# Optimization experiments

Measured on AMD Instinct MI355X. Metric: run time of the kernel, lower is better.

Reference implementation:

```python
import jax, jax.numpy as jnp
import numpy as np

B, Q, D, H, HD, LP, M = 16, 1, 2048, 16, 128, 2048, 8192
EPS = 1e-5

def _ln(x, w, b):
    mu = jnp.mean(x, axis=-1, keepdims=True)
    var = jnp.mean((x - mu) ** 2, axis=-1, keepdims=True)
    return (x - mu) * jax.lax.rsqrt(var + EPS) * w + b

def setup_inputs() -> dict:
    key = jax.random.key(0)
    ks = jax.random.split(key, 8)
    std = 0.02
    return {
        "input": jax.random.normal(ks[0], (B, Q, D), jnp.float32),
        "past_key": jax.random.normal(ks[1], (B, LP, H, HD), jnp.float32),
        "past_value": jax.random.normal(ks[2], (B, LP, H, HD), jnp.float32),
        "ln0_w": jnp.ones((D,), jnp.float32),
        "ln0_b": jnp.zeros((D,), jnp.float32),
        "ln1_w": jnp.ones((D,), jnp.float32),
        "ln1_b": jnp.zeros((D,), jnp.float32),
        "wqkv": jax.random.normal(ks[3], (3 * D, D), jnp.float32) * std,
        "wo": jax.random.normal(ks[4], (D, D), jnp.float32) * std,
        "fc0_w": jax.random.normal(ks[5], (M, D), jnp.float32) * std,
        "fc0_b": jnp.zeros((M,), jnp.float32),
        "fc1_w": jax.random.normal(ks[6], (D, M), jnp.float32) * std,
        "fc1_b": jnp.zeros((D,), jnp.float32),
    }

def reference(input, past_key, past_value, ln0_w, ln0_b, ln1_w, ln1_b,
              wqkv, wo, fc0_w, fc0_b, fc1_w, fc1_b):
    # norm0 + fused QKV projection (no bias)
    x = _ln(input, ln0_w, ln0_b)                       # [B,Q,D]
    qkv = (x @ wqkv.T).reshape(B, Q, 3, H, HD)
    q, k, v = qkv[:, :, 0], qkv[:, :, 1], qkv[:, :, 2]  # each [B,Q,H,HD]
    # append to KV cache
    k = jnp.concatenate([past_key, k], axis=1)          # [B,LP+Q,H,HD]
    v = jnp.concatenate([past_value, v], axis=1)
    # decode attention; q_len == 1 so no causal mask is applied (matches source)
    scores = jnp.einsum('nqhd,nkhd->nhqk', q, k) / (HD ** 0.5)
    attn = jax.nn.softmax(scores.astype(jnp.float32), axis=-1).astype(scores.dtype)
    attn_out = jnp.einsum('nhql,nlhd->nqhd', attn, v).reshape(B, Q, D)
    attn_out = attn_out @ wo.T
    h = input + attn_out
    # MLP2 with exact (erf) GELU as in torch F.gelu
    y = _ln(h, ln1_w, ln1_b)
    y = jax.nn.gelu(y @ fc0_w.T + fc0_b, approximate=False) @ fc1_w.T + fc1_b
    return h + y
```

## Files before the change

### kernel.cpp

```cpp
#include <hip/hip_runtime.h>
#include <math.h>

typedef __attribute__((ext_vector_type(4))) float f32x4;
typedef __attribute__((ext_vector_type(4))) _Float16 f16x4;

#define B_  16
#define D_  2048
#define H_  16
#define HD_ 128
#define LP_ 2048
#define M_  8192
#define QKV_R (3 * D_)
#define SCALE 0.08838834764831845f
#define NSPLIT 64
#define KPS 32

__device__ inline float wave_sum(float v) {
  for (int m = 32; m > 0; m >>= 1) v += __shfl_xor(v, m);
  return v;
}

__global__ void ln_kernel(const float* __restrict__ x, const float* __restrict__ w,
                          const float* __restrict__ bb, float* __restrict__ o) {
  __shared__ float sred[4];
  int b = blockIdx.x, t = threadIdx.x;
  const float* xr = x + (size_t)b * D_;
  f32x4 v0 = *(const f32x4*)(xr + t * 8);
  f32x4 v1 = *(const f32x4*)(xr + t * 8 + 4);
  float s = (v0[0] + v0[1] + v0[2] + v0[3]) + (v1[0] + v1[1] + v1[2] + v1[3]);
  s = wave_sum(s);
  if ((t & 63) == 0) sred[t >> 6] = s;
  __syncthreads();
  float mu = (sred[0] + sred[1] + sred[2] + sred[3]) * (1.0f / D_);
  __syncthreads();
  float sq = 0.f;
  for (int i = 0; i < 4; i++) {
    float d0 = v0[i] - mu; sq += d0 * d0;
    float d1 = v1[i] - mu; sq += d1 * d1;
  }
  sq = wave_sum(sq);
  if ((t & 63) == 0) sred[t >> 6] = sq;
  __syncthreads();
  float var = (sred[0] + sred[1] + sred[2] + sred[3]) * (1.0f / D_);
  float rs = rsqrtf(var + 1e-5f);
  f32x4 w0 = *(const f32x4*)(w + t * 8), w1 = *(const f32x4*)(w + t * 8 + 4);
  f32x4 c0 = *(const f32x4*)(bb + t * 8), c1 = *(const f32x4*)(bb + t * 8 + 4);
  f32x4 o0, o1;
  for (int i = 0; i < 4; i++) {
    o0[i] = (v0[i] - mu) * rs * w0[i] + c0[i];
    o1[i] = (v1[i] - mu) * rs * w1[i] + c1[i];
  }
  *(f32x4*)(o + (size_t)b * D_ + t * 8) = o0;
  *(f32x4*)(o + (size_t)b * D_ + t * 8 + 4) = o1;
}

__global__ void gemv_k(const float* __restrict__ W, const float* __restrict__ X,
                       float* __restrict__ part, int R, int K, int kc) {
  int wave = threadIdx.x >> 6, lane = threadIdx.x & 63;
  int j0 = (blockIdx.x * 4 + wave) * 16;
  int k0 = blockIdx.y * kc;
  int col = lane & 15;
  int kg  = (lane >> 4) << 2;
  const float* wp = W + (size_t)(j0 + col) * K + k0 + kg;
  const float* xp = X + (size_t)col * K + k0 + kg;
  f32x4 acc = {0.f, 0.f, 0.f, 0.f};
  #pragma unroll 4
  for (int kk = 0; kk < kc; kk += 16) {
    f32x4 av = *(const f32x4*)xp; xp += 16;
    f32x4 bv = *(const f32x4*)wp; wp += 16;
    f16x4 ah, bh;
    for (int i = 0; i < 4; i++) { ah[i] = (_Float16)av[i]; bh[i] = (_Float16)bv[i]; }
    acc = __builtin_amdgcn_mfma_f32_16x16x16f16(ah, bh, acc, 0, 0, 0);
  }
  *(f32x4*)(part + ((size_t)blockIdx.y * R + j0 + col) * 16 + kg) = acc;
}

__global__ void reduce_plain(const float* __restrict__ part, float* __restrict__ out,
                             int R, int S) {
  int i = blockIdx.x * 256 + threadIdx.x;
  int j = i >> 4, b = i & 15;
  float s = 0.f;
  for (int k = 0; k < S; k++) s += part[(size_t)k * R * 16 + i];
  out[(size_t)b * R + j] = s;
}
__global__ void reduce_resid(const float* __restrict__ part, const float* __restrict__ resid,
                             float* __restrict__ out, int R, int S) {
  int i = blockIdx.x * 256 + threadIdx.x;
  int j = i >> 4, b = i & 15;
  float s = 0.f;
  for (int k = 0; k < S; k++) s += part[(size_t)k * R * 16 + i];
  out[(size_t)b * R + j] = resid[(size_t)b * R + j] + s;
}
__global__ void reduce_bias_gelu(const float* __restrict__ part, const float* __restrict__ bias,
                                 float* __restrict__ out, int R, int S) {
  int i = blockIdx.x * 256 + threadIdx.x;
  int j = i >> 4, b = i & 15;
  float s = 0.f;
  for (int k = 0; k < S; k++) s += part[(size_t)k * R * 16 + i];
  float u = s + bias[j];
  out[(size_t)b * R + j] = 0.5f * u * (1.0f + erff(u * 0.70710678118654752f));
}
__global__ void reduce_bias_resid(const float* __restrict__ part, const float* __restrict__ bias,
                                  const float* __restrict__ resid, float* __restrict__ out,
                                  int R, int S) {
  int i = blockIdx.x * 256 + threadIdx.x;
  int j = i >> 4, b = i & 15;
  float s = 0.f;
  for (int k = 0; k < S; k++) s += part[(size_t)k * R * 16 + i];
  out[(size_t)b * R + j] = resid[(size_t)b * R + j] + s + bias[j];
}

__global__ void attn_scores(const float* __restrict__ qkv, const float* __restrict__ pk,
                            float* __restrict__ scores) {
  int b = blockIdx.x, split = blockIdx.y;
  int t = threadIdx.x;
  int h = t >> 4;
  __shared__ float s_t[KPS][17];
  f32x4 q0 = *(const f32x4*)(qkv + (size_t)b * QKV_R + t * 8);
  f32x4 q1 = *(const f32x4*)(qkv + (size_t)b * QKV_R + t * 8 + 4);
  for (int i = 0; i < 4; i++) { q0[i] *= SCALE; q1[i] *= SCALE; }
  const float* kb = pk + ((size_t)b * LP_ + (size_t)split * KPS) * D_ + t * 8;
  for (int l0 = 0; l0 < KPS; l0 += 8) {
    f32x4 k0[8], k1[8];
    #pragma unroll
    for (int c = 0; c < 8; c++) {
      size_t off = (size_t)(l0 + c) * D_;
      k0[c] = *(const f32x4*)(kb + off);
      k1[c] = *(const f32x4*)(kb + off + 4);
    }
    #pragma unroll
    for (int c = 0; c < 8; c++) {
      float s = q0[0]*k0[c][0] + q0[1]*k0[c][1] + q0[2]*k0[c][2] + q0[3]*k0[c][3]
              + q1[0]*k1[c][0] + q1[1]*k1[c][1] + q1[2]*k1[c][2] + q1[3]*k1[c][3];
      s += __shfl_xor(s, 1); s += __shfl_xor(s, 2);
      s += __shfl_xor(s, 4); s += __shfl_xor(s, 8);
      if ((t & 15) == 0) s_t[l0 + c][h] = s;
    }
  }
  __syncthreads();
  if ((t & 15) < 8) {
    int l4 = (t & 15) * 4;
    f32x4 o;
    for (int i = 0; i < 4; i++) o[i] = s_t[l4 + i][h];
    *(f32x4*)(scores + (size_t)(b * H_ + h) * LP_ + (size_t)split * KPS + l4) = o;
  }
}

__global__ void attn_soft(const float* __restrict__ qkv, float* __restrict__ scores,
                          float* __restrict__ pml) {
  int bh = blockIdx.x, b = bh >> 4, h = bh & 15;
  int t = threadIdx.x;
  __shared__ float sred[4];
  float prod = 0.f;
  if (t < 128) {
    float qv = qkv[(size_t)b * QKV_R + h * HD_ + t];
    float kn = qkv[(size_t)b * QKV_R + D_ + h * HD_ + t];
    prod = qv * kn;
  }
  prod = wave_sum(prod);
  if ((t & 63) == 0) sred[t >> 6] = prod;
  __syncthreads();
  float s_new = (sred[0] + sred[1] + sred[2] + sred[3]) * SCALE;
  __syncthreads();
  float* sp = scores + (size_t)bh * LP_;
  f32x4 v0 = *(const f32x4*)(sp + t * 8);
  f32x4 v1 = *(const f32x4*)(sp + t * 8 + 4);
  float m = s_new;
  for (int i = 0; i < 4; i++) m = fmaxf(m, fmaxf(v0[i], v1[i]));
  for (int mm = 32; mm > 0; mm >>= 1) m = fmaxf(m, __shfl_xor(m, mm));
  if ((t & 63) == 0) sred[t >> 6] = m;
  __syncthreads();
  float M = fmaxf(fmaxf(sred[0], sred[1]), fmaxf(sred[2], sred[3]));
  __syncthreads();
  float ls = 0.f;
  for (int i = 0; i < 4; i++) {
    v0[i] = __expf(v0[i] - M); ls += v0[i];
    v1[i] = __expf(v1[i] - M); ls += v1[i];
  }
  ls = wave_sum(ls);
  if ((t & 63) == 0) sred[t >> 6] = ls;
  __syncthreads();
  float en = __expf(s_new - M);
  float L = sred[0] + sred[1] + sred[2] + sred[3] + en;
  float inv = 1.0f / L;
  for (int i = 0; i < 4; i++) { v0[i] *= inv; v1[i] *= inv; }
  *(f32x4*)(sp + t * 8) = v0;
  *(f32x4*)(sp + t * 8 + 4) = v1;
  if (t == 0) pml[bh] = en * inv;
}

__global__ void attn_av(const float* __restrict__ scores, const float* __restrict__ pv,
                        float* __restrict__ pacc) {
  int b = blockIdx.x, split = blockIdx.y;
  int t = threadIdx.x, h = t >> 4;
  const float* vb = pv + ((size_t)b * LP_ + (size_t)split * KPS) * D_ + t * 8;
  const float* pp = scores + (size_t)(b * H_ + h) * LP_ + (size_t)split * KPS;
  f32x4 a0 = {0.f, 0.f, 0.f, 0.f}, a1 = {0.f, 0.f, 0.f, 0.f};
  for (int l0 = 0; l0 < KPS; l0 += 8) {
    f32x4 p0 = *(const f32x4*)(pp + l0);
    f32x4 p1 = *(const f32x4*)(pp + l0 + 4);
    f32x4 w0[8], w1[8];
    #pragma unroll
    for (int c = 0; c < 8; c++) {
      size_t off = (size_t)(l0 + c) * D_;
      w0[c] = *(const f32x4*)(vb + off);
      w1[c] = *(const f32x4*)(vb + off + 4);
    }
    #pragma unroll
    for (int c = 0; c < 8; c++) {
      float p = (c < 4) ? p0[c] : p1[c - 4];
      for (int i = 0; i < 4; i++) { a0[i] += p * w0[c][i]; a1[i] += p * w1[c][i]; }
    }
  }
  size_t oi = (((size_t)b * NSPLIT + split) * H_ + h) * HD_ + (t & 15) * 8;
  *(f32x4*)(pacc + oi) = a0;
  *(f32x4*)(pacc + oi + 4) = a1;
}

__global__ void attn_comb(const float* __restrict__ qkv, const float* __restrict__ pml,
                          const float* __restrict__ pacc, float* __restrict__ attn_out) {
  int bh = blockIdx.x, b = bh >> 4, h = bh & 15;
  int t = threadIdx.x;
  float o = 0.f;
  for (int s = 0; s < NSPLIT; s++)
    o += pacc[(((size_t)b * NSPLIT + s) * H_ + h) * HD_ + t];
  o += pml[bh] * qkv[(size_t)b * QKV_R + 2 * D_ + h * HD_ + t];
  attn_out[(size_t)b * D_ + h * HD_ + t] = o;
}

extern "C" void kernel_launch(void* const* d_in, const int* in_sizes, int n_in,
                              void* d_out, int out_size, void* d_ws, size_t ws_size,
                              hipStream_t stream) {
  const float* input  = (const float*)d_in[0];
  const float* pk     = (const float*)d_in[1];
  const float* pv     = (const float*)d_in[2];
  const float* ln0_w  = (const float*)d_in[3];
  const float* ln0_b  = (const float*)d_in[4];
  const float* ln1_w  = (const float*)d_in[5];
  const float* ln1_b  = (const float*)d_in[6];
  const float* wqkv   = (const float*)d_in[7];
  const float* wo     = (const float*)d_in[8];
  const float* fc0_w  = (const float*)d_in[9];
  const float* fc0_b  = (const float*)d_in[10];
  const float* fc1_w  = (const float*)d_in[11];
  const float* fc1_b  = (const float*)d_in[12];
  float* out = (float*)d_out;

  char* wsb = (char*)d_ws;
  float* x_ln     = (float*)(wsb + 0);
  float* qkv      = (float*)(wsb + 131072);
  float* attn_out = (float*)(wsb + 524288);
  float* hbuf     = (float*)(wsb + 655360);
  float* y0       = (float*)(wsb + 786432);
  float* act      = (float*)(wsb + 917504);
  float* scores   = (float*)(wsb + 1441792);
  float* pml      = (float*)(wsb + 3538944);
  float* pacc     = (float*)(wsb + 3543040);
  float* part     = (float*)(wsb + 11931648);

  ln_kernel<<<16, 256, 0, stream>>>(input, ln0_w, ln0_b, x_ln);
  gemv_k<<<dim3(96, 8), 256, 0, stream>>>(wqkv, x_ln, part, QKV_R, D_, 256);
  reduce_plain<<<384, 256, 0, stream>>>(part, qkv, QKV_R, 8);
  attn_scores<<<dim3(B_, NSPLIT), 256, 0, stream>>>(qkv, pk, scores);
  attn_soft<<<256, 256, 0, stream>>>(qkv, scores, pml);
  attn_av<<<dim3(B_, NSPLIT), 256, 0, stream>>>(scores, pv, pacc);
  attn_comb<<<256, 128, 0, stream>>>(qkv, pml, pacc, attn_out);
  gemv_k<<<dim3(32, 16), 256, 0, stream>>>(wo, attn_out, part, D_, D_, 128);
  reduce_resid<<<128, 256, 0, stream>>>(part, input, hbuf, D_, 16);
  ln_kernel<<<16, 256, 0, stream>>>(hbuf, ln1_w, ln1_b, y0);
  gemv_k<<<dim3(128, 4), 256, 0, stream>>>(fc0_w, y0, part, M_, D_, 512);
  reduce_bias_gelu<<<512, 256, 0, stream>>>(part, fc0_b, act, M_, 4);
  gemv_k<<<dim3(32, 16), 256, 0, stream>>>(fc1_w, act, part, D_, M_, 512);
  reduce_bias_resid<<<128, 256, 0, stream>>>(part, fc1_b, hbuf, out, D_, 16);
}
```

Measured before the change: 211.1 us.

## Double-buffer KV tiles into LDS via direct global-to-LDS loads in attention

The attention score and AV kernels now stream K/V rows into LDS with global_load_lds in a two-stage double buffer. Each stage holds two rows, and explicit vmcnt waits and barriers overlap the next tile's load with compute on the current one. The split count is halved and keys per split doubled, which halves the number of blocks and partial accumulators. The cost is more LDS per block and a barrier per tile, which may reduce occupancy and add synchronisation overhead compared with the old register-prefetch of eight rows.

```diff
diff --git a/kernel.cpp b/kernel.cpp
--- a/kernel.cpp
+++ b/kernel.cpp
@@ -12,12 +12,20 @@
 #define M_  8192
 #define QKV_R (3 * D_)
 #define SCALE 0.08838834764831845f
-#define NSPLIT 64
-#define KPS 32
+#define NSPLIT 32
+#define KPS 64
+#define TROWS 2
+#define NT (KPS / TROWS)
 
 __device__ inline float wave_sum(float v) {
   for (int m = 32; m > 0; m >>= 1) v += __shfl_xor(v, m);
   return v;
+}
+
+__device__ inline void gl_lds16(const float* g, float* l) {
+  __builtin_amdgcn_global_load_lds(
+      (const __attribute__((address_space(1))) void*)g,
+      (__attribute__((address_space(3))) void*)l, 16, 0, 0);
 }
 
 __global__ void ln_kernel(const float* __restrict__ x, const float* __restrict__ w,
@@ -112,37 +120,59 @@
 
 __global__ void attn_scores(const float* __restrict__ qkv, const float* __restrict__ pk,
                             float* __restrict__ scores) {
-  int b = blockIdx.x, split = blockIdx.y;
+  int b = blockIdx.x, sp = blockIdx.y;
   int t = threadIdx.x;
-  int h = t >> 4;
-  __shared__ float s_t[KPS][17];
-  f32x4 q0 = *(const f32x4*)(qkv + (size_t)b * QKV_R + t * 8);
-  f32x4 q1 = *(const f32x4*)(qkv + (size_t)b * QKV_R + t * 8 + 4);
+  int wv = __builtin_amdgcn_readfirstlane(threadIdx.x) >> 6;
+  int lane = t & 63;
+  int h = t >> 4, d8 = (t & 15) * 8;
+  __shared__ float kbuf[2][TROWS][D_];
+  __shared__ float s_t[H_][KPS + 1];
+
+  f32x4 q0 = *(const f32x4*)(qkv + (size_t)b * QKV_R + h * HD_ + d8);
+  f32x4 q1 = *(const f32x4*)(qkv + (size_t)b * QKV_R + h * HD_ + d8 + 4);
   for (int i = 0; i < 4; i++) { q0[i] *= SCALE; q1[i] *= SCALE; }
-  const float* kb = pk + ((size_t)b * LP_ + (size_t)split * KPS) * D_ + t * 8;
-  for (int l0 = 0; l0 < KPS; l0 += 8) {
-    f32x4 k0[8], k1[8];
+
+  const float* gbase = pk + ((size_t)b * LP_ + (size_t)sp * KPS) * D_;
+  auto stage = [&](int buf, int tile) {
+    const float* src = gbase + (size_t)tile * (TROWS * D_) + wv * 1024 + lane * 4;
+    float* dst = &kbuf[buf][0][0] + wv * 1024;
     #pragma unroll
-    for (int c = 0; c < 8; c++) {
-      size_t off = (size_t)(l0 + c) * D_;
-      k0[c] = *(const f32x4*)(kb + off);
-      k1[c] = *(const f32x4*)(kb + off + 4);
+    for (int j = 0; j < 4; j++) gl_lds16(src + j * 256, dst + j * 256);
+  };
+
+  stage(0, 0);
+  for (int tile = 0; tile < NT; ++tile) {
+    int cur = tile & 1;
+    if (tile + 1 < NT) {
+      stage(cur ^ 1, tile + 1);
+      __builtin_amdgcn_sched_barrier(0);
+      asm volatile("s_waitcnt vmcnt(4)" ::: "memory");
+    } else {
+      __builtin_amdgcn_sched_barrier(0);
+      asm volatile("s_waitcnt vmcnt(0)" ::: "memory");
     }
+    __builtin_amdgcn_s_barrier();
+    __builtin_amdgcn_sched_barrier(0);
     #pragma unroll
-    for (int c = 0; c < 8; c++) {
-      float s = q0[0]*k0[c][0] + q0[1]*k0[c][1] + q0[2]*k0[c][2] + q0[3]*k0[c][3]
-              + q1[0]*k1[c][0] + q1[1]*k1[c][1] + q1[2]*k1[c][2] + q1[3]*k1[c][3];
+    for (int r = 0; r < TROWS; ++r) {
+      const float* kr = &kbuf[cur][r][h * HD_ + d8];
+      f32x4 k0 = *(const f32x4*)kr;
+      f32x4 k1 = *(const f32x4*)(kr + 4);
+      float s = q0[0]*k0[0] + q0[1]*k0[1] + q0[2]*k0[2] + q0[3]*k0[3]
+              + q1[0]*k1[0] + q1[1]*k1[1] + q1[2]*k1[2] + q1[3]*k1[3];
       s += __shfl_xor(s, 1); s += __shfl_xor(s, 2);
       s += __shfl_xor(s, 4); s += __shfl_xor(s, 8);
-      if ((t & 15) == 0) s_t[l0 + c][h] = s;
+      if ((t & 15) == 0) s_t[h][tile * TROWS + r] = s;
     }
-  }
-  __syncthreads();
-  if ((t & 15) < 8) {
+    asm volatile("" ::: "memory");
+    __builtin_amdgcn_s_barrier();
+  }
+  __syncthreads();
+  {
     int l4 = (t & 15) * 4;
     f32x4 o;
-    for (int i = 0; i < 4; i++) o[i] = s_t[l4 + i][h];
-    *(f32x4*)(scores + (size_t)(b * H_ + h) * LP_ + (size_t)split * KPS + l4) = o;
+    for (int i = 0; i < 4; i++) o[i] = s_t[h][l4 + i];
+    *(f32x4*)(scores + (size_t)(b * H_ + h) * LP_ + (size_t)sp * KPS + l4) = o;
   }
 }
 
@@ -191,28 +221,56 @@
 
 __global__ void attn_av(const float* __restrict__ scores, const float* __restrict__ pv,
                         float* __restrict__ pacc) {
-  int b = blockIdx.x, split = blockIdx.y;
-  int t = threadIdx.x, h = t >> 4;
-  const float* vb = pv + ((size_t)b * LP_ + (size_t)split * KPS) * D_ + t * 8;
-  const float* pp = scores + (size_t)(b * H_ + h) * LP_ + (size_t)split * KPS;
+  int b = blockIdx.x, sp = blockIdx.y;
+  int t = threadIdx.x;
+  int wv = __builtin_amdgcn_readfirstlane(threadIdx.x) >> 6;
+  int lane = t & 63;
+  int h = t >> 4, d8 = (t & 15) * 8;
+  __shared__ float vbuf[2][TROWS][D_];
+  __shared__ float p_l[H_][KPS + 1];
+
+  {
+    int l4 = (t & 15) * 4;
+    f32x4 pr = *(const f32x4*)(scores + (size_t)(b * H_ + h) * LP_ + (size_t)sp * KPS + l4);
+    for (int i = 0; i < 4; i++) p_l[h][l4 + i] = pr[i];
+  }
+
+  const float* gbase = pv + ((size_t)b * LP_ + (size_t)sp * KPS) * D_;
+  auto stage = [&](int buf, int tile) {
+    const float* src = gbase + (size_t)tile * (TROWS * D_) + wv * 1024 + lane * 4;
+    float* dst = &vbuf[buf][0][0] + wv * 1024;
+    #pragma unroll
+    for (int j = 0; j < 4; j++) gl_lds16(src + j * 256, dst + j * 256);
+  };
+
+  stage(0, 0);
+  __syncthreads();
+
   f32x4 a0 = {0.f, 0.f, 0.f, 0.f}, a1 = {0.f, 0.f, 0.f, 0.f};
-  for (int l0 = 0; l0 < KPS; l0 += 8) {
-    f32x4 p0 = *(const f32x4*)(pp + l0);
-    f32x4 p1 = *(const f32x4*)(pp + l0 + 4);
-    f32x4 w0[8], w1[8];
+  for (int tile = 0; tile < NT; ++tile) {
+    int cur = tile & 1;
+    if (tile + 1 < NT) {
+      stage(cur ^ 1, tile + 1);
+      __builtin_amdgcn_sched_barrier(0);
+      asm volatile("s_waitcnt vmcnt(4)" ::: "memory");
+    } else {
+      __builtin_amdgcn_sched_barrier(0);
+      asm volatile("s_waitcnt vmcnt(0)" ::: "memory");
+    }
+    __builtin_amdgcn_s_barrier();
+    __builtin_amdgcn_sched_barrier(0);
     #pragma unroll
-    for (int c = 0; c < 8; c++) {
-      size_t off = (size_t)(l0 + c) * D_;
-      w0[c] = *(const f32x4*)(vb + off);
-      w1[c] = *(const f32x4*)(vb + off + 4);
+    for (int r = 0; r < TROWS; ++r) {
+      float p = p_l[h][tile * TROWS + r];
+      const float* vr = &vbuf[cur][r][h * HD_ + d8];
+      f32x4 v0 = *(const f32x4*)vr;
+      f32x4 v1 = *(const f32x4*)(vr + 4);
+      for (int i = 0; i < 4; i++) { a0[i] += p * v0[i]; a1[i] += p * v1[i]; }
     }
-    #pragma unroll
-    for (int c = 0; c < 8; c++) {
-      float p = (c < 4) ? p0[c] : p1[c - 4];
-      for (int i = 0; i < 4; i++) { a0[i] += p * w0[c][i]; a1[i] += p * w1[c][i]; }
-    }
-  }
-  size_t oi = (((size_t)b * NSPLIT + split) * H_ + h) * HD_ + (t & 15) * 8;
+    asm volatile("" ::: "memory");
+    __builtin_amdgcn_s_barrier();
+  }
+  size_t oi = (((size_t)b * NSPLIT + sp) * H_ + h) * HD_ + d8;
   *(f32x4*)(pacc + oi) = a0;
   *(f32x4*)(pacc + oi + 4) = a1;
 }
```

Measured after the change: 197.4 us. -6.5%, faster.

## Pipeline K/V streaming through swizzled LDS ring with async global-to-LDS loads

Applied to the files above, without the earlier changes.

The attention score and AV kernels now run as single-wave blocks. Each block streams its 32 K or V rows through a 4-deep LDS ring filled by direct global-to-LDS loads, with explicit vmcnt waits keeping three rows in flight. An XOR swizzle lets each lane read its contiguous 32-float slice without bank conflicts, and the head reduction shrinks to two shuffles. The goal is more memory-level parallelism while streaming the KV cache. The trade-offs are 32KB of LDS per 64-thread block, which caps how many waves fit on a CU, and fragile hand-written waitcnt logic.

```diff
diff --git a/kernel.cpp b/kernel.cpp
--- a/kernel.cpp
+++ b/kernel.cpp
@@ -13,11 +13,35 @@
 #define QKV_R (3 * D_)
 #define SCALE 0.08838834764831845f
 #define NSPLIT 64
-#define KPS 32
+#define KPW 32
+#define DEPTH 4
 
 __device__ inline float wave_sum(float v) {
   for (int m = 32; m > 0; m >>= 1) v += __shfl_xor(v, m);
   return v;
+}
+
+__device__ inline void gl_lds16(const float* g, float* l) {
+  __builtin_amdgcn_global_load_lds(
+      (const __attribute__((address_space(1))) void*)g,
+      (__attribute__((address_space(3))) void*)l, 16, 0, 0);
+}
+
+__device__ inline void stage_row(const float* rowbase, float* ringrow, int lane) {
+  #pragma unroll
+  for (int j = 0; j < 8; j++) {
+    int x  = j * 1024 + lane * 16;
+    int sx = x ^ (((x >> 7) & 7) << 4);
+    gl_lds16(rowbase + (sx >> 2), ringrow + j * 256);
+  }
+}
+
+__device__ inline void read_row(const float* ringrow, int lane, f32x4 kv[8]) {
+  #pragma unroll
+  for (int j = 0; j < 8; j++) {
+    int fo = lane * 32 + ((j ^ (lane & 7)) << 2);
+    kv[j] = *(const f32x4*)(ringrow + fo);
+  }
 }
 
 __global__ void ln_kernel(const float* __restrict__ x, const float* __restrict__ w,
@@ -112,37 +136,52 @@
 
 __global__ void attn_scores(const float* __restrict__ qkv, const float* __restrict__ pk,
                             float* __restrict__ scores) {
-  int b = blockIdx.x, split = blockIdx.y;
-  int t = threadIdx.x;
-  int h = t >> 4;
-  __shared__ float s_t[KPS][17];
-  f32x4 q0 = *(const f32x4*)(qkv + (size_t)b * QKV_R + t * 8);
-  f32x4 q1 = *(const f32x4*)(qkv + (size_t)b * QKV_R + t * 8 + 4);
-  for (int i = 0; i < 4; i++) { q0[i] *= SCALE; q1[i] *= SCALE; }
-  const float* kb = pk + ((size_t)b * LP_ + (size_t)split * KPS) * D_ + t * 8;
-  for (int l0 = 0; l0 < KPS; l0 += 8) {
-    f32x4 k0[8], k1[8];
+  int b = blockIdx.x, sp = blockIdx.y;
+  int lane = threadIdx.x;
+  __shared__ float ring[DEPTH][D_];
+  __shared__ float s_t[H_][KPW + 1];
+
+  f32x4 q[8];
+  #pragma unroll
+  for (int j = 0; j < 8; j++) {
+    q[j] = *(const f32x4*)(qkv + (size_t)b * QKV_R + lane * 32 + j * 4);
+    for (int i = 0; i < 4; i++) q[j][i] *= SCALE;
+  }
+
+  const float* gbase = pk + ((size_t)b * LP_ + (size_t)sp * KPW) * D_;
+  stage_row(gbase + 0 * D_, ring[0], lane);
+  stage_row(gbase + 1 * D_, ring[1], lane);
+  stage_row(gbase + 2 * D_, ring[2], lane);
+
+  for (int r = 0; r < KPW; ++r) {
+    if (r + 3 < KPW) {
+      stage_row(gbase + (size_t)(r + 3) * D_, ring[(r + 3) & (DEPTH - 1)], lane);
+      __builtin_amdgcn_sched_barrier(0);
+      asm volatile("s_waitcnt vmcnt(24)" ::: "memory");
+    } else if (r == KPW - 3) {
+      asm volatile("s_waitcnt vmcnt(16)" ::: "memory");
+    } else if (r == KPW - 2) {
+      asm volatile("s_waitcnt vmcnt(8)" ::: "memory");
+    } else {
+      asm volatile("s_waitcnt vmcnt(0)" ::: "memory");
+    }
+    __builtin_amdgcn_sched_barrier(0);
+    f32x4 kv[8];
+    read_row(ring[r & (DEPTH - 1)], lane, kv);
+    float s = 0.f;
     #pragma unroll
-    for (int c = 0; c < 8; c++) {
-      size_t off = (size_t)(l0 + c) * D_;
-      k0[c] = *(const f32x4*)(kb + off);
-      k1[c] = *(const f32x4*)(kb + off + 4);
-    }
-    #pragma unroll
-    for (int c = 0; c < 8; c++) {
-      float s = q0[0]*k0[c][0] + q0[1]*k0[c][1] + q0[2]*k0[c][2] + q0[3]*k0[c][3]
-              + q1[0]*k1[c][0] + q1[1]*k1[c][1] + q1[2]*k1[c][2] + q1[3]*k1[c][3];
-      s += __shfl_xor(s, 1); s += __shfl_xor(s, 2);
-      s += __shfl_xor(s, 4); s += __shfl_xor(s, 8);
-      if ((t & 15) == 0) s_t[l0 + c][h] = s;
-    }
-  }
-  __syncthreads();
-  if ((t & 15) < 8) {
-    int l4 = (t & 15) * 4;
+    for (int j = 0; j < 8; j++)
+      s += q[j][0]*kv[j][0] + q[j][1]*kv[j][1] + q[j][2]*kv[j][2] + q[j][3]*kv[j][3];
+    s += __shfl_xor(s, 1);
+    s += __shfl_xor(s, 2);
+    if ((lane & 3) == 0) s_t[lane >> 2][r] = s;
+  }
+  #pragma unroll
+  for (int half = 0; half < 2; half++) {
+    int h = lane >> 2, i4 = (lane & 3) * 4 + half * 16;
     f32x4 o;
-    for (int i = 0; i < 4; i++) o[i] = s_t[l4 + i][h];
-    *(f32x4*)(scores + (size_t)(b * H_ + h) * LP_ + (size_t)split * KPS + l4) = o;
+    for (int i = 0; i < 4; i++) o[i] = s_t[h][i4 + i];
+    *(f32x4*)(scores + (size_t)(b * H_ + h) * LP_ + (size_t)sp * KPW + i4) = o;
   }
 }
 
@@ -191,30 +230,51 @@
 
 __global__ void attn_av(const float* __restrict__ scores, const float* __restrict__ pv,
                         float* __restrict__ pacc) {
-  int b = blockIdx.x, split = blockIdx.y;
-  int t = threadIdx.x, h = t >> 4;
-  const float* vb = pv + ((size_t)b * LP_ + (size_t)split * KPS) * D_ + t * 8;
-  const float* pp = scores + (size_t)(b * H_ + h) * LP_ + (size_t)split * KPS;
-  f32x4 a0 = {0.f, 0.f, 0.f, 0.f}, a1 = {0.f, 0.f, 0.f, 0.f};
-  for (int l0 = 0; l0 < KPS; l0 += 8) {
-    f32x4 p0 = *(const f32x4*)(pp + l0);
-    f32x4 p1 = *(const f32x4*)(pp + l0 + 4);
-    f32x4 w0[8], w1[8];
+  int b = blockIdx.x, sp = blockIdx.y;
+  int lane = threadIdx.x;
+  __shared__ float ring[DEPTH][D_];
+  __shared__ float p_l[H_][KPW + 1];
+
+  #pragma unroll
+  for (int half = 0; half < 2; half++) {
+    int h = lane >> 2, i4 = (lane & 3) * 4 + half * 16;
+    f32x4 pr = *(const f32x4*)(scores + (size_t)(b * H_ + h) * LP_ + (size_t)sp * KPW + i4);
+    for (int i = 0; i < 4; i++) p_l[h][i4 + i] = pr[i];
+  }
+
+  const float* gbase = pv + ((size_t)b * LP_ + (size_t)sp * KPW) * D_;
+  stage_row(gbase + 0 * D_, ring[0], lane);
+  stage_row(gbase + 1 * D_, ring[1], lane);
+  stage_row(gbase + 2 * D_, ring[2], lane);
+
+  int h = lane >> 2;
+  f32x4 a[8];
+  #pragma unroll
+  for (int j = 0; j < 8; j++) a[j] = (f32x4){0.f, 0.f, 0.f, 0.f};
+
+  for (int r = 0; r < KPW; ++r) {
+    if (r + 3 < KPW) {
+      stage_row(gbase + (size_t)(r + 3) * D_, ring[(r + 3) & (DEPTH - 1)], lane);
+      __builtin_amdgcn_sched_barrier(0);
+      asm volatile("s_waitcnt vmcnt(24)" ::: "memory");
+    } else if (r == KPW - 3) {
+      asm volatile("s_waitcnt vmcnt(16)" ::: "memory");
+    } else if (r == KPW - 2) {
+      asm volatile("s_waitcnt vmcnt(8)" ::: "memory");
+    } else {
+      asm volatile("s_waitcnt vmcnt(0)" ::: "memory");
+    }
+    __builtin_amdgcn_sched_barrier(0);
+    f32x4 kv[8];
+    read_row(ring[r & (DEPTH - 1)], lane, kv);
+    float p = p_l[h][r];
     #pragma unroll
-    for (int c = 0; c < 8; c++) {
-      size_t off = (size_t)(l0 + c) * D_;
-      w0[c] = *(const f32x4*)(vb + off);
-      w1[c] = *(const f32x4*)(vb + off + 4);
-    }
-    #pragma unroll
-    for (int c = 0; c < 8; c++) {
-      float p = (c < 4) ? p0[c] : p1[c - 4];
-      for (int i = 0; i < 4; i++) { a0[i] += p * w0[c][i]; a1[i] += p * w1[c][i]; }
-    }
-  }
-  size_t oi = (((size_t)b * NSPLIT + split) * H_ + h) * HD_ + (t & 15) * 8;
-  *(f32x4*)(pacc + oi) = a0;
-  *(f32x4*)(pacc + oi + 4) = a1;
+    for (int j = 0; j < 8; j++)
+      for (int i = 0; i < 4; i++) a[j][i] += p * kv[j][i];
+  }
+  float* ob = pacc + (((size_t)b * NSPLIT + sp) * H_ + h) * HD_ + (lane & 3) * 32;
+  #pragma unroll
+  for (int j = 0; j < 8; j++) *(f32x4*)(ob + j * 4) = a[j];
 }
 
 __global__ void attn_comb(const float* __restrict__ qkv, const float* __restrict__ pml,
@@ -261,9 +321,9 @@
   ln_kernel<<<16, 256, 0, stream>>>(input, ln0_w, ln0_b, x_ln);
   gemv_k<<<dim3(96, 8), 256, 0, stream>>>(wqkv, x_ln, part, QKV_R, D_, 256);
   reduce_plain<<<384, 256, 0, stream>>>(part, qkv, QKV_R, 8);
-  attn_scores<<<dim3(B_, NSPLIT), 256, 0, stream>>>(qkv, pk, scores);
+  attn_scores<<<dim3(B_, NSPLIT), 64, 0, stream>>>(qkv, pk, scores);
   attn_soft<<<256, 256, 0, stream>>>(qkv, scores, pml);
-  attn_av<<<dim3(B_, NSPLIT), 256, 0, stream>>>(scores, pv, pacc);
+  attn_av<<<dim3(B_, NSPLIT), 64, 0, stream>>>(scores, pv, pacc);
   attn_comb<<<256, 128, 0, stream>>>(qkv, pml, pacc, attn_out);
   gemv_k<<<dim3(32, 16), 256, 0, stream>>>(wo, attn_out, part, D_, D_, 128);
   reduce_resid<<<128, 256, 0, stream>>>(part, input, hbuf, D_, 16);
```

After: 207.1 us. No clear change (-1.9%).
